# Performance work log

Measured on AMD Instinct MI355X. Metric: run time of the kernel, lower is better.

The kernel has to match this reference:

```python
import jax, jax.numpy as jnp
import numpy as np


def setup_inputs() -> dict:
    key = jax.random.key(0)
    k1, k2, k3 = jax.random.split(key, 3)
    B, S, D, O, C = 4, 1024, 1024, 1024, 8
    x = jax.random.normal(k1, (B, S, D), dtype=jnp.float32)
    category_id = jax.random.randint(k2, (B, S), 0, C, dtype=jnp.int64)
    weight = jax.random.normal(k3, (C, D, O), dtype=jnp.float32)
    bias = jnp.zeros((C, O), dtype=jnp.float32)
    return {"x": x, "category_id": category_id, "weight": weight, "bias": bias}


def reference(x, category_id, weight, bias):
    # Faithful to: out[t] = x[t] @ weight[cid[t]] + bias[cid[t]]
    # Instead of gathering a full [T, D, O] per-token weight tensor (the torch
    # original's bmm formulation), compute x against every category's matrix and
    # select the row for each token's category -- same math, far less memory.
    orig_shape = x.shape
    T = np.prod(orig_shape[:-1])
    x_flat = x.reshape(T, orig_shape[-1])            # [T, D]
    cid = category_id.reshape(T)                      # [T]
    y_all = jnp.einsum('td,cdo->tco', x_flat, weight)  # [T, C, O]
    y = jnp.take_along_axis(y_all, cid[:, None, None], axis=1)[:, 0, :]  # [T, O]
    out = y + bias[cid]                               # [T, O]
    return out.reshape(*orig_shape[:-1], out.shape[-1])
```

## Files before the change

### kernel.cpp

```cpp
#include <hip/hip_runtime.h>


typedef __attribute__((ext_vector_type(8))) short bf16x8;
typedef __attribute__((ext_vector_type(4))) float f32x4;
typedef __attribute__((ext_vector_type(8))) unsigned short ushort8_t;

__device__ __forceinline__ unsigned short f2bf(float f) {
  unsigned u = __float_as_uint(f);
  u += 0x7FFFu + ((u >> 16) & 1u);
  return (unsigned short)(u >> 16);
}

__device__ __forceinline__ void gload_lds16(const unsigned short* g, unsigned short* l) {
  __builtin_amdgcn_global_load_lds(
      (const __attribute__((address_space(1))) unsigned int*)g,
      (__attribute__((address_space(3))) unsigned int*)l, 16, 0, 0);
}

#define MAXC 8

__global__ void k_prep(const float* __restrict__ W, unsigned short* __restrict__ Wt,
                       int Dd, int Oo,
                       const float* __restrict__ x, unsigned short* __restrict__ xb, int nX,
                       const int* __restrict__ cid, int* __restrict__ counts,
                       int* __restrict__ bucket, int T, int C, int tpw) {
  int b   = blockIdx.x;
  int tid = threadIdx.x;

  if (b == 0) {
    __shared__ int cnt[256][MAXC];
    int tpt = (T + 255) / 256;
    int t0  = tid * tpt;
    int t1  = min(t0 + tpt, T);
    for (int c = 0; c < C; ++c) cnt[tid][c] = 0;
    for (int t = t0; t < t1; ++t) cnt[tid][cid[t]]++;
    __syncthreads();
    if (tid < C) {
      int run = 0;
      for (int t = 0; t < 256; ++t) { int v = cnt[t][tid]; cnt[t][tid] = run; run += v; }
      counts[tid] = run;
    }
    __syncthreads();
    for (int t = t0; t < t1; ++t) {
      int c = cid[t];
      int p = cnt[tid][c]++;
      bucket[c * T + p] = t;
    }
    return;
  }

  if (b > tpw) {
    int i = ((b - tpw - 1) * 256 + tid) * 8;
    if (i >= nX) return;
    float4 a0 = *reinterpret_cast<const float4*>(x + i);
    float4 a1 = *reinterpret_cast<const float4*>(x + i + 4);
    ushort8_t o;
    o[0] = f2bf(a0.x); o[1] = f2bf(a0.y); o[2] = f2bf(a0.z); o[3] = f2bf(a0.w);
    o[4] = f2bf(a1.x); o[5] = f2bf(a1.y); o[6] = f2bf(a1.z); o[7] = f2bf(a1.w);
    *reinterpret_cast<ushort8_t*>(xb + i) = o;
    return;
  }

  int bb  = b - 1;
  int tpc = (Dd / 64) * (Oo / 64);
  int c   = bb / tpc;
  int rem = bb % tpc;
  int d0  = (rem / (Oo / 64)) * 64;
  int o0  = (rem % (Oo / 64)) * 64;

  __shared__ float t[64][65];
  const float* Wc = W + (size_t)c * Dd * Oo;
#pragma unroll
  for (int p = 0; p < 4; ++p) {
    int chunk = p * 256 + tid;
    int r  = chunk >> 4;
    int cb = chunk & 15;
    float4 v = *reinterpret_cast<const float4*>(Wc + (size_t)(d0 + r) * Oo + o0 + cb * 4);
    t[r][cb * 4 + 0] = v.x; t[r][cb * 4 + 1] = v.y;
    t[r][cb * 4 + 2] = v.z; t[r][cb * 4 + 3] = v.w;
  }
  __syncthreads();
  unsigned short* Wtc = Wt + (size_t)c * Oo * Dd;
#pragma unroll
  for (int p = 0; p < 2; ++p) {
    int chunk = p * 256 + tid;
    int orow = chunk >> 3;
    int dseg = chunk & 7;
    ushort8_t w;
#pragma unroll
    for (int j = 0; j < 8; ++j) w[j] = f2bf(t[dseg * 8 + j][orow]);
    *reinterpret_cast<ushort8_t*>(Wtc + (size_t)(o0 + orow) * Dd + d0 + dseg * 8) = w;
  }
}

#define BM 64
#define BN 128
#define BK 64
#define TILE_A (BM * BK)
#define TILE_B (BN * BK)

__global__ __launch_bounds__(512) void k_ggemm(
    const unsigned short* __restrict__ xb, const unsigned short* __restrict__ Wt,
    const float* __restrict__ bias, const int* __restrict__ counts,
    const int* __restrict__ bucket, float* __restrict__ out,
    int T, int Dd, int Oo) {
  int c  = blockIdx.x;
  int Mc = counts[c];
  int m0 = blockIdx.z * BM;
  if (m0 >= Mc) return;
  int n0 = blockIdx.y * BN;

  extern __shared__ __align__(16) unsigned short smem[];
  unsigned short* Al = smem;
  unsigned short* Bl = smem + 3 * TILE_A;

  const int tid  = threadIdx.x;
  const int lane = tid & 63;
  const int wid  = tid >> 6;
  const int wm   = wid >> 2, wn = wid & 3;

  const int* buck = bucket + c * T;
  const unsigned short* Wc = Wt + (size_t)c * Oo * Dd;

  const unsigned short* aSrc;
  const unsigned short* bSrc[2];
  int aOff, bOff[2];
  {
    int row = wid * 8 + (lane >> 3);
    int seg = (lane & 7) ^ (row & 7);
    int mr  = m0 + row;
    int tok = buck[mr < Mc ? mr : Mc - 1];
    aSrc = xb + (size_t)tok * Dd + seg * 8;
    aOff = (wid * 8) * BK;
  }
#pragma unroll
  for (int i = 0; i < 2; ++i) {
    int row = wid * 16 + i * 8 + (lane >> 3);
    int seg = (lane & 7) ^ (row & 7);
    bSrc[i] = Wc + (size_t)(n0 + row) * Dd + seg * 8;
    bOff[i] = (wid * 16 + i * 8) * BK;
  }

  const f32x4 fzero = {0.f, 0.f, 0.f, 0.f};
  f32x4 acc[2][2];
#pragma unroll
  for (int i = 0; i < 2; ++i)
#pragma unroll
    for (int j = 0; j < 2; ++j) acc[i][j] = fzero;

  const int KT = Dd / BK;

#pragma unroll
  for (int t8 = 0; t8 < 2; ++t8) {
    unsigned short* Ab = Al + t8 * TILE_A;
    unsigned short* Bb = Bl + t8 * TILE_B;
    int ko = t8 * BK;
    gload_lds16(aSrc + ko, Ab + aOff);
#pragma unroll
    for (int i = 0; i < 2; ++i) gload_lds16(bSrc[i] + ko, Bb + bOff[i]);
  }

  int cur = 0;
  for (int kt = 0; kt < KT; ++kt) {
    asm volatile("s_waitcnt lgkmcnt(0)" ::: "memory");
    if (kt < KT - 1) {
      asm volatile("s_waitcnt vmcnt(3)" ::: "memory");
    } else {
      asm volatile("s_waitcnt vmcnt(0)" ::: "memory");
    }
    __builtin_amdgcn_sched_barrier(0);
    __builtin_amdgcn_s_barrier();
    __builtin_amdgcn_sched_barrier(0);

    if (kt + 2 < KT) {
      int nb = cur + 2; if (nb >= 3) nb -= 3;
      int ko = (kt + 2) * BK;
      unsigned short* An = Al + nb * TILE_A;
      unsigned short* Bn = Bl + nb * TILE_B;
      gload_lds16(aSrc + ko, An + aOff);
#pragma unroll
      for (int i = 0; i < 2; ++i) gload_lds16(bSrc[i] + ko, Bn + bOff[i]);
    }

    const unsigned short* Ac = Al + cur * TILE_A;
    const unsigned short* Bc = Bl + cur * TILE_B;
#pragma unroll
    for (int kk = 0; kk < 2; ++kk) {
      bf16x8 af[2], bf[2];
#pragma unroll
      for (int mi = 0; mi < 2; ++mi) {
        int row  = wm * 32 + mi * 16 + (lane & 15);
        int slot = (kk * 4 + (lane >> 4)) ^ (row & 7);
        af[mi] = *reinterpret_cast<const bf16x8*>(&Ac[row * BK + slot * 8]);
      }
#pragma unroll
      for (int ni = 0; ni < 2; ++ni) {
        int row  = wn * 32 + ni * 16 + (lane & 15);
        int slot = (kk * 4 + (lane >> 4)) ^ (row & 7);
        bf[ni] = *reinterpret_cast<const bf16x8*>(&Bc[row * BK + slot * 8]);
      }
      __builtin_amdgcn_s_setprio(1);
#pragma unroll
      for (int mi = 0; mi < 2; ++mi)
#pragma unroll
        for (int ni = 0; ni < 2; ++ni)
          acc[mi][ni] = __builtin_amdgcn_mfma_f32_16x16x32_bf16(af[mi], bf[ni], acc[mi][ni], 0, 0, 0);
      __builtin_amdgcn_s_setprio(0);
    }
    cur = (cur + 1 == 3) ? 0 : cur + 1;
  }

#pragma unroll
  for (int mi = 0; mi < 2; ++mi) {
    int rb = m0 + wm * 32 + mi * 16 + (lane >> 4) * 4;
#pragma unroll
    for (int r = 0; r < 4; ++r) {
      int mrow = rb + r;
      if (mrow < Mc) {
        int tok = buck[mrow];
        float* orow = out + (size_t)tok * Oo;
#pragma unroll
        for (int ni = 0; ni < 2; ++ni) {
          int col = n0 + wn * 32 + ni * 16 + (lane & 15);
          orow[col] = acc[mi][ni][r] + bias[c * Oo + col];
        }
      }
    }
  }
}

extern "C" void kernel_launch(void* const* d_in, const int* in_sizes, int n_in,
                              void* d_out, int out_size, void* d_ws, size_t ws_size,
                              hipStream_t stream) {
  const float* x    = (const float*)d_in[0];
  const int*   cid  = (const int*)d_in[1];
  const float* W    = (const float*)d_in[2];
  const float* bias = (const float*)d_in[3];
  float* out = (float*)d_out;

  int T = in_sizes[1];
  int D = in_sizes[0] / T;
  int O = out_size / T;
  int C = in_sizes[3] / O;

  char* ws = (char*)d_ws;
  int* counts = (int*)ws;
  int* bucket = (int*)(ws + 64);
  unsigned short* xb = (unsigned short*)(ws + 64 + (size_t)C * T * 4);
  unsigned short* Wt = xb + (size_t)T * D;

  int tpw  = C * (D / 64) * (O / 64);
  int cvtb = (T * D / 8 + 255) / 256;
  k_prep<<<1 + tpw + cvtb, 256, 0, stream>>>(W, Wt, D, O, x, xb, T * D,
                                             cid, counts, bucket, T, C, tpw);
  size_t ldsBytes = (size_t)3 * (TILE_A + TILE_B) * sizeof(unsigned short);
  k_ggemm<<<dim3(C, O / BN, (T + BM - 1) / BM), 512, ldsBytes, stream>>>(
      xb, Wt, bias, counts, bucket, out, T, D, O);
}
```

Measured before the change: 48.40 us.

## Shrink grouped GEMM M tile to 32 with double-buffered static LDS

Halves the M tile of the grouped GEMM from 64 to 32 rows, so there are more blocks per category to fill the GPU. The three-stage prefetch pipeline becomes a two-buffer scheme in static LDS with a full vmcnt(0) wait and barrier every k-step. The warp layout changes so each wave covers all 32 rows and one 16-column slice, and launch bounds now request higher occupancy. The trade-off is that each block reuses loaded weight tiles across fewer rows, doubling B-tile traffic, and the shallower pipeline exposes more global load latency.

New measurement: 59.10 us. 1.22x slower.

```diff
diff --git a/kernel.cpp b/kernel.cpp
--- a/kernel.cpp
+++ b/kernel.cpp
@@ -93,13 +93,13 @@
   }
 }
 
-#define BM 64
+#define BM 32
 #define BN 128
 #define BK 64
 #define TILE_A (BM * BK)
 #define TILE_B (BN * BK)
 
-__global__ __launch_bounds__(512) void k_ggemm(
+__global__ __launch_bounds__(512, 8) void k_ggemm(
     const unsigned short* __restrict__ xb, const unsigned short* __restrict__ Wt,
     const float* __restrict__ bias, const int* __restrict__ counts,
     const int* __restrict__ bucket, float* __restrict__ out,
@@ -110,29 +110,28 @@
   if (m0 >= Mc) return;
   int n0 = blockIdx.y * BN;
 
-  extern __shared__ __align__(16) unsigned short smem[];
-  unsigned short* Al = smem;
-  unsigned short* Bl = smem + 3 * TILE_A;
+  __shared__ __align__(16) unsigned short Al[2][TILE_A];
+  __shared__ __align__(16) unsigned short Bl[2][TILE_B];
 
   const int tid  = threadIdx.x;
   const int lane = tid & 63;
   const int wid  = tid >> 6;
-  const int wm   = wid >> 2, wn = wid & 3;
 
   const int* buck = bucket + c * T;
   const unsigned short* Wc = Wt + (size_t)c * Oo * Dd;
 
   const unsigned short* aSrc;
-  const unsigned short* bSrc[2];
-  int aOff, bOff[2];
+  int aOff;
   {
-    int row = wid * 8 + (lane >> 3);
+    int row = wid * 4 + (lane >> 3);
     int seg = (lane & 7) ^ (row & 7);
-    int mr  = m0 + row;
+    int mr  = m0 + (row & 31);
     int tok = buck[mr < Mc ? mr : Mc - 1];
     aSrc = xb + (size_t)tok * Dd + seg * 8;
-    aOff = (wid * 8) * BK;
-  }
+    aOff = (wid * 4) * BK;
+  }
+  const unsigned short* bSrc[2];
+  int bOff[2];
 #pragma unroll
   for (int i = 0; i < 2; ++i) {
     int row = wid * 16 + i * 8 + (lane >> 3);
@@ -142,88 +141,63 @@
   }
 
   const f32x4 fzero = {0.f, 0.f, 0.f, 0.f};
-  f32x4 acc[2][2];
-#pragma unroll
-  for (int i = 0; i < 2; ++i)
-#pragma unroll
-    for (int j = 0; j < 2; ++j) acc[i][j] = fzero;
+  f32x4 acc[2];
+  acc[0] = fzero; acc[1] = fzero;
 
   const int KT = Dd / BK;
 
-#pragma unroll
-  for (int t8 = 0; t8 < 2; ++t8) {
-    unsigned short* Ab = Al + t8 * TILE_A;
-    unsigned short* Bb = Bl + t8 * TILE_B;
-    int ko = t8 * BK;
-    gload_lds16(aSrc + ko, Ab + aOff);
-#pragma unroll
-    for (int i = 0; i < 2; ++i) gload_lds16(bSrc[i] + ko, Bb + bOff[i]);
-  }
-
-  int cur = 0;
+  if (lane < 32) gload_lds16(aSrc, &Al[0][aOff]);
+#pragma unroll
+  for (int i = 0; i < 2; ++i) gload_lds16(bSrc[i], &Bl[0][bOff[i]]);
+  asm volatile("s_waitcnt vmcnt(0)" ::: "memory");
+  __builtin_amdgcn_sched_barrier(0);
+  __builtin_amdgcn_s_barrier();
+
   for (int kt = 0; kt < KT; ++kt) {
-    asm volatile("s_waitcnt lgkmcnt(0)" ::: "memory");
-    if (kt < KT - 1) {
-      asm volatile("s_waitcnt vmcnt(3)" ::: "memory");
-    } else {
-      asm volatile("s_waitcnt vmcnt(0)" ::: "memory");
-    }
-    __builtin_amdgcn_sched_barrier(0);
-    __builtin_amdgcn_s_barrier();
-    __builtin_amdgcn_sched_barrier(0);
-
-    if (kt + 2 < KT) {
-      int nb = cur + 2; if (nb >= 3) nb -= 3;
-      int ko = (kt + 2) * BK;
-      unsigned short* An = Al + nb * TILE_A;
-      unsigned short* Bn = Bl + nb * TILE_B;
-      gload_lds16(aSrc + ko, An + aOff);
-#pragma unroll
-      for (int i = 0; i < 2; ++i) gload_lds16(bSrc[i] + ko, Bn + bOff[i]);
-    }
-
-    const unsigned short* Ac = Al + cur * TILE_A;
-    const unsigned short* Bc = Bl + cur * TILE_B;
+    int cur = kt & 1;
+    if (kt + 1 < KT) {
+      int ko = (kt + 1) * BK;
+      int nb = cur ^ 1;
+      if (lane < 32) gload_lds16(aSrc + ko, &Al[nb][aOff]);
+#pragma unroll
+      for (int i = 0; i < 2; ++i) gload_lds16(bSrc[i] + ko, &Bl[nb][bOff[i]]);
+    }
 #pragma unroll
     for (int kk = 0; kk < 2; ++kk) {
-      bf16x8 af[2], bf[2];
+      bf16x8 af[2], bf;
 #pragma unroll
       for (int mi = 0; mi < 2; ++mi) {
-        int row  = wm * 32 + mi * 16 + (lane & 15);
+        int row  = mi * 16 + (lane & 15);
         int slot = (kk * 4 + (lane >> 4)) ^ (row & 7);
-        af[mi] = *reinterpret_cast<const bf16x8*>(&Ac[row * BK + slot * 8]);
+        af[mi] = *reinterpret_cast<const bf16x8*>(&Al[cur][row * BK + slot * 8]);
       }
-#pragma unroll
-      for (int ni = 0; ni < 2; ++ni) {
-        int row  = wn * 32 + ni * 16 + (lane & 15);
+      {
+        int row  = wid * 16 + (lane & 15);
         int slot = (kk * 4 + (lane >> 4)) ^ (row & 7);
-        bf[ni] = *reinterpret_cast<const bf16x8*>(&Bc[row * BK + slot * 8]);
+        bf = *reinterpret_cast<const bf16x8*>(&Bl[cur][row * BK + slot * 8]);
       }
       __builtin_amdgcn_s_setprio(1);
-#pragma unroll
-      for (int mi = 0; mi < 2; ++mi)
-#pragma unroll
-        for (int ni = 0; ni < 2; ++ni)
-          acc[mi][ni] = __builtin_amdgcn_mfma_f32_16x16x32_bf16(af[mi], bf[ni], acc[mi][ni], 0, 0, 0);
+      acc[0] = __builtin_amdgcn_mfma_f32_16x16x32_bf16(af[0], bf, acc[0], 0, 0, 0);
+      acc[1] = __builtin_amdgcn_mfma_f32_16x16x32_bf16(af[1], bf, acc[1], 0, 0, 0);
       __builtin_amdgcn_s_setprio(0);
     }
-    cur = (cur + 1 == 3) ? 0 : cur + 1;
+    if (kt + 1 < KT) {
+      asm volatile("s_waitcnt vmcnt(0)" ::: "memory");
+      __builtin_amdgcn_sched_barrier(0);
+      __builtin_amdgcn_s_barrier();
+    }
   }
 
 #pragma unroll
   for (int mi = 0; mi < 2; ++mi) {
-    int rb = m0 + wm * 32 + mi * 16 + (lane >> 4) * 4;
+    int rb = m0 + mi * 16 + (lane >> 4) * 4;
 #pragma unroll
     for (int r = 0; r < 4; ++r) {
       int mrow = rb + r;
       if (mrow < Mc) {
         int tok = buck[mrow];
-        float* orow = out + (size_t)tok * Oo;
-#pragma unroll
-        for (int ni = 0; ni < 2; ++ni) {
-          int col = n0 + wn * 32 + ni * 16 + (lane & 15);
-          orow[col] = acc[mi][ni][r] + bias[c * Oo + col];
-        }
+        int col = n0 + wid * 16 + (lane & 15);
+        out[(size_t)tok * Oo + col] = acc[mi][r] + bias[c * Oo + col];
       }
     }
   }
@@ -253,7 +227,6 @@
   int cvtb = (T * D / 8 + 255) / 256;
   k_prep<<<1 + tpw + cvtb, 256, 0, stream>>>(W, Wt, D, O, x, xb, T * D,
                                              cid, counts, bucket, T, C, tpw);
-  size_t ldsBytes = (size_t)3 * (TILE_A + TILE_B) * sizeof(unsigned short);
-  k_ggemm<<<dim3(C, O / BN, (T + BM - 1) / BM), 512, ldsBytes, stream>>>(
+  k_ggemm<<<dim3(C, O / BN, (T + BM - 1) / BM), 512, 0, stream>>>(
       xb, Wt, bias, counts, bucket, out, T, D, O);
 }
```
